# Optimization experiments

Hardware: AMD Instinct MI355X
Metric: run time of the kernel (lower is better)

The kernel has to match this reference:

```python
import jax, jax.numpy as jnp
import numpy as np

LEVELS = 2048
TIMESTAMPS = 64
D = 32768
SIG_LO, SIG_HI = -5.0, 5.0
FEAT_IDX = jnp.array([557, 581, 553, 551, 92, 554, 579, 570, 573, 577, 565, 286, 555, 549, 13, 550, 63, 580, 556, 564, 0, 576, 567, 552, 578, 588, 597, 566, 571, 44, 572, 574, 14, 582, 381, 594, 4, 593, 218, 25, 84, 592, 3, 591, 547, 561, 562, 548, 319, 596, 558, 563, 87, 65, 599, 17, 88, 2, 49, 309, 6, 81, 15, 590, 589, 43, 273, 420, 546, 568, 400, 277, 202, 287, 434, 435, 423, 431, 301, 417, 412, 205, 179, 327, 176, 442, 172, 450, 391, 163, 154, 480, 485, 490, 491, 498, 503, 507, 509, 452, 239, 388, 219, 303, 292, 310, 316, 320, 322, 324, 326, 330, 336, 263, 262, 339, 340, 256, 345, 347], dtype=jnp.int32)


def _bipolar(k, shape):
    # torchhd MAP hypervectors are random +/-1
    return jnp.where(jax.random.bernoulli(k, 0.5, shape), 1.0, -1.0).astype(jnp.float32)


def _level_idx(x, low, high, n):
    # torchhd value_to_index: linear map of [low, high] onto {0, ..., n-1}
    return jnp.clip(jnp.round((x - low) / (high - low) * (n - 1)), 0, n - 1).astype(jnp.int32)


def setup_inputs() -> dict:
    key = jax.random.key(0)
    ks = jax.random.split(key, 7)
    inp = jax.random.normal(ks[0], (TIMESTAMPS, 4), dtype=jnp.float32) * 2.0
    feat = jax.random.normal(ks[1], (600,), dtype=jnp.float32)
    Wx = _bipolar(ks[2], (LEVELS, D))
    Wy = _bipolar(ks[3], (LEVELS, D))
    Wz = _bipolar(ks[4], (LEVELS, D))
    Wt = _bipolar(ks[5], (TIMESTAMPS, D))
    keys = _bipolar(ks[6], (120, D))
    return {"input": inp, "feat": feat, "Wx": Wx, "Wy": Wy, "Wz": Wz, "Wt": Wt, "keys": keys}


def reference(input, feat, Wx, Wy, Wz, Wt, keys):
    # Level-embedding lookups for the clamped x/y/z accelerometer signals
    xl = Wx[_level_idx(jnp.clip(input[:, 1], SIG_LO, SIG_HI), SIG_LO, SIG_HI, LEVELS)]  # [W, D]
    yl = Wy[_level_idx(jnp.clip(input[:, 2], SIG_LO, SIG_HI), SIG_LO, SIG_HI, LEVELS)]
    zl = Wz[_level_idx(jnp.clip(input[:, 3], SIG_LO, SIG_HI), SIG_LO, SIG_HI, LEVELS)]
    window = input.shape[0]
    t = jnp.arange(window, dtype=jnp.float32)
    tl = Wt[_level_idx(t, 0.0, float(TIMESTAMPS), TIMESTAMPS)]  # [W, D]
    sample_hvs = (xl + yl + zl) * tl                            # [W, D]
    sample_hv = jnp.prod(sample_hvs, axis=0)                    # multibind -> [D]
    # DensityFlocet: key-value binding of 120 gathered features with thermometer (flocet) value codes
    fv = jnp.clip(feat[FEAT_IDX], -1.0, 1.0)                    # [120]
    fidx = jnp.round((fv + 1.0) * 0.5 * D).astype(jnp.int32)    # threshold per feature
    therm = jnp.where(jnp.arange(D)[None, :] < fidx[:, None], 1.0, -1.0)  # [120, D]
    feat_hv = jnp.sum(keys * therm, axis=0)                     # multiset(bind) -> [D]
    combined = sample_hv + feat_hv + sample_hv * feat_hv
    return jnp.where(combined > 0, 1.0, -1.0).reshape(-1)       # hard_quantize + flatten
```

## Files before the change

kernel.cpp:

```cpp
#include <hip/hip_runtime.h>

#define D_DIM 32768
#define NT 64
#define NKEYS 120
#define TPB 1024
#define DB 128
#define NW 16

__constant__ int c_feat_idx[NKEYS] = {
    557, 581, 553, 551, 92, 554, 579, 570, 573, 577,
    565, 286, 555, 549, 13, 550, 63, 580, 556, 564,
    0, 576, 567, 552, 578, 588, 597, 566, 571, 44,
    572, 574, 14, 582, 381, 594, 4, 593, 218, 25,
    84, 592, 3, 591, 547, 561, 562, 548, 319, 596,
    558, 563, 87, 65, 599, 17, 88, 2, 49, 309,
    6, 81, 15, 590, 589, 43, 273, 420, 546, 568,
    400, 277, 202, 287, 434, 435, 423, 431, 301, 417,
    412, 205, 179, 327, 176, 442, 172, 450, 391, 163,
    154, 480, 485, 490, 491, 498, 503, 507, 509, 452,
    239, 388, 219, 303, 292, 310, 316, 320, 322, 324,
    326, 330, 336, 263, 262, 339, 340, 256, 345, 347};

__device__ __forceinline__ int level_idx(float x) {
    x = fminf(fmaxf(x, -5.0f), 5.0f);
    float v = (x + 5.0f) / 10.0f * 2047.0f;
    int i = (int)rintf(v);
    return min(max(i, 0), 2047);
}

__global__ __launch_bounds__(TPB) void hdc_encode_kernel(
    const float* __restrict__ input,
    const float* __restrict__ feat,
    const float* __restrict__ Wx,
    const float* __restrict__ Wy,
    const float* __restrict__ Wz,
    const float* __restrict__ Wt,
    const float* __restrict__ keys,
    float* __restrict__ out)
{
    __shared__ int   s_idx[4][NT];
    __shared__ int   s_fidx[NKEYS];
    __shared__ int   s_meta[NW][DB];
    __shared__ float s_f[NW][DB];

    const int tid = threadIdx.x;

    if (tid < NT) {
        float x = input[tid * 4 + 1];
        float y = input[tid * 4 + 2];
        float z = input[tid * 4 + 3];
        s_idx[0][tid] = level_idx(x);
        s_idx[1][tid] = level_idx(y);
        s_idx[2][tid] = level_idx(z);
        float tv = (float)tid;
        int it = (int)rintf(tv / 64.0f * 63.0f);
        s_idx[3][tid] = min(max(it, 0), NT - 1);
    } else if (tid < NT + NKEYS) {
        int j = tid - NT;
        float fv = feat[c_feat_idx[j]];
        fv = fminf(fmaxf(fv, -1.0f), 1.0f);
        s_fidx[j] = (int)rintf((fv + 1.0f) * 0.5f * 32768.0f);
    }
    __syncthreads();

    const int wave = __builtin_amdgcn_readfirstlane(tid >> 6);
    const int lane = tid & 63;
    const int d0 = blockIdx.x * DB + lane * 2;

    unsigned sg0 = 0u, sg1 = 0u;
    int a30 = 0, a31 = 0;
    const int t0 = wave * 4;
#pragma unroll
    for (int k = 0; k < 4; ++k) {
        int t = t0 + k;
        int ix = __builtin_amdgcn_readfirstlane(s_idx[0][t]);
        int iy = __builtin_amdgcn_readfirstlane(s_idx[1][t]);
        int iz = __builtin_amdgcn_readfirstlane(s_idx[2][t]);
        int it = __builtin_amdgcn_readfirstlane(s_idx[3][t]);
        float2 x = *(const float2*)(Wx + ((size_t)ix << 15) + d0);
        float2 y = *(const float2*)(Wy + ((size_t)iy << 15) + d0);
        float2 z = *(const float2*)(Wz + ((size_t)iz << 15) + d0);
        float2 w = *(const float2*)(Wt + ((size_t)it << 15) + d0);
        float sA = x.x + y.x + z.x;
        float sB = x.y + y.y + z.y;
        sg0 ^= __float_as_uint(sA * w.x);
        sg1 ^= __float_as_uint(sB * w.y);
        a30 |= (fabsf(sA) > 2.0f) ? 1 : 0;
        a31 |= (fabsf(sB) > 2.0f) ? 1 : 0;
    }

    float f0 = 0.0f, f1 = 0.0f;
    if (wave < 8) {
        const int j0 = wave * 8;
#pragma unroll
        for (int k = 0; k < 8; ++k) {
            int j = j0 + k;
            int fx = __builtin_amdgcn_readfirstlane(s_fidx[j]);
            float2 kv = *(const float2*)(keys + ((size_t)j << 15) + d0);
            f0 += (d0 < fx) ? kv.x : -kv.x;
            f1 += (d0 + 1 < fx) ? kv.y : -kv.y;
        }
    } else {
        const int j0 = 64 + (wave - 8) * 7;
#pragma unroll
        for (int k = 0; k < 7; ++k) {
            int j = j0 + k;
            int fx = __builtin_amdgcn_readfirstlane(s_fidx[j]);
            float2 kv = *(const float2*)(keys + ((size_t)j << 15) + d0);
            f0 += (d0 < fx) ? kv.x : -kv.x;
            f1 += (d0 + 1 < fx) ? kv.y : -kv.y;
        }
    }

    const int col = lane * 2;
    s_meta[wave][col]     = (int)(sg0 >> 31) | (a30 << 8);
    s_meta[wave][col + 1] = (int)(sg1 >> 31) | (a31 << 8);
    s_f[wave][col]     = f0;
    s_f[wave][col + 1] = f1;
    __syncthreads();

    if (tid < DB) {
        int msum = 0;
        float f = 0.0f;
#pragma unroll
        for (int w2 = 0; w2 < NW; ++w2) {
            msum += s_meta[w2][tid];
            f    += s_f[w2][tid];
        }
        bool neg  = (msum & 1) != 0;
        bool any3 = (msum & 0xFF00) != 0;
        float o;
        if (f >= 0.0f) o = neg ? -1.0f : 1.0f;
        else           o = (neg && any3) ? 1.0f : -1.0f;
        out[blockIdx.x * DB + tid] = o;
    }
}

extern "C" void kernel_launch(void* const* d_in, const int* in_sizes, int n_in,
                              void* d_out, int out_size, void* d_ws, size_t ws_size,
                              hipStream_t stream) {
    const float* input = (const float*)d_in[0];
    const float* feat  = (const float*)d_in[1];
    const float* Wx    = (const float*)d_in[2];
    const float* Wy    = (const float*)d_in[3];
    const float* Wz    = (const float*)d_in[4];
    const float* Wt    = (const float*)d_in[5];
    const float* keys  = (const float*)d_in[6];
    float* out = (float*)d_out;

    dim3 grid(D_DIM / DB);
    dim3 block(TPB);
    hipLaunchKernelGGL(hdc_encode_kernel, grid, block, 0, stream,
                       input, feat, Wx, Wy, Wz, Wt, keys, out);
}
```

Before: 13.79 us.

## Compute indices per wave in registers and batch all gathers before arithmetic

Removes the shared-memory index precompute stage and its barrier: each wave now computes its own level and threshold indices directly from global input. All row loads for the embedding and key tables are issued up front into register arrays before any accumulation, so more memory requests are in flight at once. In exchange, index arithmetic and the small input and feature reads are repeated by every wave of every block, and register pressure rises.

New measurement: 14.84 us. 1.08x slower.

```diff
diff --git a/kernel.cpp b/kernel.cpp
--- a/kernel.cpp
+++ b/kernel.cpp
@@ -38,77 +38,77 @@
     const float* __restrict__ keys,
     float* __restrict__ out)
 {
-    __shared__ int   s_idx[4][NT];
-    __shared__ int   s_fidx[NKEYS];
     __shared__ int   s_meta[NW][DB];
     __shared__ float s_f[NW][DB];
 
-    const int tid = threadIdx.x;
-
-    if (tid < NT) {
-        float x = input[tid * 4 + 1];
-        float y = input[tid * 4 + 2];
-        float z = input[tid * 4 + 3];
-        s_idx[0][tid] = level_idx(x);
-        s_idx[1][tid] = level_idx(y);
-        s_idx[2][tid] = level_idx(z);
-        float tv = (float)tid;
-        int it = (int)rintf(tv / 64.0f * 63.0f);
-        s_idx[3][tid] = min(max(it, 0), NT - 1);
-    } else if (tid < NT + NKEYS) {
-        int j = tid - NT;
-        float fv = feat[c_feat_idx[j]];
-        fv = fminf(fmaxf(fv, -1.0f), 1.0f);
-        s_fidx[j] = (int)rintf((fv + 1.0f) * 0.5f * 32768.0f);
-    }
-    __syncthreads();
-
+    const int tid  = threadIdx.x;
     const int wave = __builtin_amdgcn_readfirstlane(tid >> 6);
     const int lane = tid & 63;
     const int d0 = blockIdx.x * DB + lane * 2;
 
+    int rowx[4], rowy[4], rowz[4], rowt[4];
+#pragma unroll
+    for (int k = 0; k < 4; ++k) {
+        int t = wave * 4 + k;
+        float x = input[t * 4 + 1];
+        float y = input[t * 4 + 2];
+        float z = input[t * 4 + 3];
+        rowx[k] = __builtin_amdgcn_readfirstlane(level_idx(x));
+        rowy[k] = __builtin_amdgcn_readfirstlane(level_idx(y));
+        rowz[k] = __builtin_amdgcn_readfirstlane(level_idx(z));
+        float tv = (float)t;
+        int it = (int)rintf(tv / 64.0f * 63.0f);
+        rowt[k] = __builtin_amdgcn_readfirstlane(min(max(it, 0), NT - 1));
+    }
+
+    const int nk = (wave < 8) ? 8 : 7;
+    const int j0 = (wave < 8) ? wave * 8 : 64 + (wave - 8) * 7;
+    int fxv[8];
+#pragma unroll
+    for (int k = 0; k < 8; ++k) {
+        if (k < nk) {
+            float fv = feat[c_feat_idx[j0 + k]];
+            fv = fminf(fmaxf(fv, -1.0f), 1.0f);
+            fxv[k] = __builtin_amdgcn_readfirstlane((int)rintf((fv + 1.0f) * 0.5f * 32768.0f));
+        } else {
+            fxv[k] = 0;
+        }
+    }
+
+    float2 sx[4], sy[4], sz[4], st[4];
+#pragma unroll
+    for (int k = 0; k < 4; ++k) {
+        sx[k] = *(const float2*)(Wx + ((size_t)rowx[k] << 15) + d0);
+        sy[k] = *(const float2*)(Wy + ((size_t)rowy[k] << 15) + d0);
+        sz[k] = *(const float2*)(Wz + ((size_t)rowz[k] << 15) + d0);
+        st[k] = *(const float2*)(Wt + ((size_t)rowt[k] << 15) + d0);
+    }
+    float2 kv[8];
+#pragma unroll
+    for (int k = 0; k < 8; ++k) {
+        if (k < nk)
+            kv[k] = *(const float2*)(keys + ((size_t)(j0 + k) << 15) + d0);
+    }
+
     unsigned sg0 = 0u, sg1 = 0u;
     int a30 = 0, a31 = 0;
-    const int t0 = wave * 4;
 #pragma unroll
     for (int k = 0; k < 4; ++k) {
-        int t = t0 + k;
-        int ix = __builtin_amdgcn_readfirstlane(s_idx[0][t]);
-        int iy = __builtin_amdgcn_readfirstlane(s_idx[1][t]);
-        int iz = __builtin_amdgcn_readfirstlane(s_idx[2][t]);
-        int it = __builtin_amdgcn_readfirstlane(s_idx[3][t]);
-        float2 x = *(const float2*)(Wx + ((size_t)ix << 15) + d0);
-        float2 y = *(const float2*)(Wy + ((size_t)iy << 15) + d0);
-        float2 z = *(const float2*)(Wz + ((size_t)iz << 15) + d0);
-        float2 w = *(const float2*)(Wt + ((size_t)it << 15) + d0);
-        float sA = x.x + y.x + z.x;
-        float sB = x.y + y.y + z.y;
-        sg0 ^= __float_as_uint(sA * w.x);
-        sg1 ^= __float_as_uint(sB * w.y);
+        float sA = sx[k].x + sy[k].x + sz[k].x;
+        float sB = sx[k].y + sy[k].y + sz[k].y;
+        sg0 ^= __float_as_uint(sA * st[k].x);
+        sg1 ^= __float_as_uint(sB * st[k].y);
         a30 |= (fabsf(sA) > 2.0f) ? 1 : 0;
         a31 |= (fabsf(sB) > 2.0f) ? 1 : 0;
     }
 
     float f0 = 0.0f, f1 = 0.0f;
-    if (wave < 8) {
-        const int j0 = wave * 8;
 #pragma unroll
-        for (int k = 0; k < 8; ++k) {
-            int j = j0 + k;
-            int fx = __builtin_amdgcn_readfirstlane(s_fidx[j]);
-            float2 kv = *(const float2*)(keys + ((size_t)j << 15) + d0);
-            f0 += (d0 < fx) ? kv.x : -kv.x;
-            f1 += (d0 + 1 < fx) ? kv.y : -kv.y;
-        }
-    } else {
-        const int j0 = 64 + (wave - 8) * 7;
-#pragma unroll
-        for (int k = 0; k < 7; ++k) {
-            int j = j0 + k;
-            int fx = __builtin_amdgcn_readfirstlane(s_fidx[j]);
-            float2 kv = *(const float2*)(keys + ((size_t)j << 15) + d0);
-            f0 += (d0 < fx) ? kv.x : -kv.x;
-            f1 += (d0 + 1 < fx) ? kv.y : -kv.y;
+    for (int k = 0; k < 8; ++k) {
+        if (k < nk) {
+            int fx = fxv[k];
+            f0 += (d0 < fx)     ? kv[k].x : -kv[k].x;
+            f1 += (d0 + 1 < fx) ? kv[k].y : -kv[k].y;
         }
     }
 
```

## Split reduction across four blocks per chunk with a separate combine kernel

Applied to the files above, without the earlier changes.

Each 128-column chunk is now processed by four 512-thread blocks, each covering 16 timestamps and 30 keys. Their partial sign/count and feature sums go to workspace, and a second kernel combines them and quantizes. Each wave computes its level indices directly instead of through a shared-memory prologue and barrier, which removes one sync. This raises block count and occupancy, at the cost of an extra kernel launch and a workspace write/read round trip. The any3 flag becomes a count so partial results can be added together.

Result: slower. 15.88 us (+15.2%).

```diff
diff --git a/kernel.cpp b/kernel.cpp
--- a/kernel.cpp
+++ b/kernel.cpp
@@ -3,9 +3,10 @@
 #define D_DIM 32768
 #define NT 64
 #define NKEYS 120
-#define TPB 1024
-#define DB 128
-#define NW 16
+#define RS 4
+#define CHUNK 128
+#define K1_TPB 512
+#define K1_WAVES 8
 
 __constant__ int c_feat_idx[NKEYS] = {
     557, 581, 553, 551, 92, 554, 579, 570, 573, 577,
@@ -28,7 +29,7 @@
     return min(max(i, 0), 2047);
 }
 
-__global__ __launch_bounds__(TPB) void hdc_encode_kernel(
+__global__ __launch_bounds__(K1_TPB, 8) void hdc_partial_kernel(
     const float* __restrict__ input,
     const float* __restrict__ feat,
     const float* __restrict__ Wx,
@@ -36,78 +37,59 @@
     const float* __restrict__ Wz,
     const float* __restrict__ Wt,
     const float* __restrict__ keys,
-    float* __restrict__ out)
+    int*   __restrict__ ws_m,
+    float* __restrict__ ws_f)
 {
-    __shared__ int   s_idx[4][NT];
-    __shared__ int   s_fidx[NKEYS];
-    __shared__ int   s_meta[NW][DB];
-    __shared__ float s_f[NW][DB];
+    __shared__ int   s_meta[K1_WAVES][CHUNK];
+    __shared__ float s_f[K1_WAVES][CHUNK];
 
-    const int tid = threadIdx.x;
+    const int tid   = threadIdx.x;
+    const int wave  = __builtin_amdgcn_readfirstlane(tid >> 6);
+    const int lane  = tid & 63;
+    const int chunk = blockIdx.x >> 2;
+    const int rg    = blockIdx.x & 3;
+    const int d0    = chunk * CHUNK + lane * 2;
 
-    if (tid < NT) {
-        float x = input[tid * 4 + 1];
-        float y = input[tid * 4 + 2];
-        float z = input[tid * 4 + 3];
-        s_idx[0][tid] = level_idx(x);
-        s_idx[1][tid] = level_idx(y);
-        s_idx[2][tid] = level_idx(z);
-        float tv = (float)tid;
-        int it = (int)rintf(tv / 64.0f * 63.0f);
-        s_idx[3][tid] = min(max(it, 0), NT - 1);
-    } else if (tid < NT + NKEYS) {
-        int j = tid - NT;
-        float fv = feat[c_feat_idx[j]];
-        fv = fminf(fmaxf(fv, -1.0f), 1.0f);
-        s_fidx[j] = (int)rintf((fv + 1.0f) * 0.5f * 32768.0f);
+    const int t0 = rg * 16 + wave * 2;
+    int rx[2], ry[2], rz[2], rt[2];
+#pragma unroll
+    for (int k = 0; k < 2; ++k) {
+        int t = t0 + k;
+        rx[k] = __builtin_amdgcn_readfirstlane(level_idx(input[t * 4 + 1]));
+        ry[k] = __builtin_amdgcn_readfirstlane(level_idx(input[t * 4 + 2]));
+        rz[k] = __builtin_amdgcn_readfirstlane(level_idx(input[t * 4 + 3]));
+        int it = (int)rintf((float)t / 64.0f * 63.0f);
+        rt[k] = __builtin_amdgcn_readfirstlane(min(max(it, 0), NT - 1));
     }
-    __syncthreads();
-
-    const int wave = __builtin_amdgcn_readfirstlane(tid >> 6);
-    const int lane = tid & 63;
-    const int d0 = blockIdx.x * DB + lane * 2;
+    const int nk = (wave < 6) ? 4 : 3;
+    const int j0 = rg * 30 + ((wave < 6) ? wave * 4 : 24 + (wave - 6) * 3);
 
     unsigned sg0 = 0u, sg1 = 0u;
     int a30 = 0, a31 = 0;
-    const int t0 = wave * 4;
 #pragma unroll
-    for (int k = 0; k < 4; ++k) {
-        int t = t0 + k;
-        int ix = __builtin_amdgcn_readfirstlane(s_idx[0][t]);
-        int iy = __builtin_amdgcn_readfirstlane(s_idx[1][t]);
-        int iz = __builtin_amdgcn_readfirstlane(s_idx[2][t]);
-        int it = __builtin_amdgcn_readfirstlane(s_idx[3][t]);
-        float2 x = *(const float2*)(Wx + ((size_t)ix << 15) + d0);
-        float2 y = *(const float2*)(Wy + ((size_t)iy << 15) + d0);
-        float2 z = *(const float2*)(Wz + ((size_t)iz << 15) + d0);
-        float2 w = *(const float2*)(Wt + ((size_t)it << 15) + d0);
+    for (int k = 0; k < 2; ++k) {
+        float2 x = *(const float2*)(Wx + ((size_t)rx[k] << 15) + d0);
+        float2 y = *(const float2*)(Wy + ((size_t)ry[k] << 15) + d0);
+        float2 z = *(const float2*)(Wz + ((size_t)rz[k] << 15) + d0);
+        float2 w = *(const float2*)(Wt + ((size_t)rt[k] << 15) + d0);
         float sA = x.x + y.x + z.x;
         float sB = x.y + y.y + z.y;
         sg0 ^= __float_as_uint(sA * w.x);
         sg1 ^= __float_as_uint(sB * w.y);
-        a30 |= (fabsf(sA) > 2.0f) ? 1 : 0;
-        a31 |= (fabsf(sB) > 2.0f) ? 1 : 0;
+        a30 += (fabsf(sA) > 2.0f) ? 1 : 0;
+        a31 += (fabsf(sB) > 2.0f) ? 1 : 0;
     }
 
     float f0 = 0.0f, f1 = 0.0f;
-    if (wave < 8) {
-        const int j0 = wave * 8;
 #pragma unroll
-        for (int k = 0; k < 8; ++k) {
+    for (int k = 0; k < 4; ++k) {
+        if (k < nk) {
             int j = j0 + k;
-            int fx = __builtin_amdgcn_readfirstlane(s_fidx[j]);
+            float fv = feat[c_feat_idx[j]];
+            fv = fminf(fmaxf(fv, -1.0f), 1.0f);
+            int fx = __builtin_amdgcn_readfirstlane((int)rintf((fv + 1.0f) * 0.5f * 32768.0f));
             float2 kv = *(const float2*)(keys + ((size_t)j << 15) + d0);
-            f0 += (d0 < fx) ? kv.x : -kv.x;
-            f1 += (d0 + 1 < fx) ? kv.y : -kv.y;
-        }
-    } else {
-        const int j0 = 64 + (wave - 8) * 7;
-#pragma unroll
-        for (int k = 0; k < 7; ++k) {
-            int j = j0 + k;
-            int fx = __builtin_amdgcn_readfirstlane(s_fidx[j]);
-            float2 kv = *(const float2*)(keys + ((size_t)j << 15) + d0);
-            f0 += (d0 < fx) ? kv.x : -kv.x;
+            f0 += (d0 < fx)     ? kv.x : -kv.x;
             f1 += (d0 + 1 < fx) ? kv.y : -kv.y;
         }
     }
@@ -119,21 +101,34 @@
     s_f[wave][col + 1] = f1;
     __syncthreads();
 
-    if (tid < DB) {
+    if (tid < CHUNK) {
         int msum = 0;
         float f = 0.0f;
 #pragma unroll
-        for (int w2 = 0; w2 < NW; ++w2) {
+        for (int w2 = 0; w2 < K1_WAVES; ++w2) {
             msum += s_meta[w2][tid];
             f    += s_f[w2][tid];
         }
-        bool neg  = (msum & 1) != 0;
-        bool any3 = (msum & 0xFF00) != 0;
-        float o;
-        if (f >= 0.0f) o = neg ? -1.0f : 1.0f;
-        else           o = (neg && any3) ? 1.0f : -1.0f;
-        out[blockIdx.x * DB + tid] = o;
+        int d = chunk * CHUNK + tid;
+        ws_m[rg * D_DIM + d] = msum;
+        ws_f[rg * D_DIM + d] = f;
     }
+}
+
+__global__ __launch_bounds__(256) void hdc_combine_kernel(
+    const int*   __restrict__ ws_m,
+    const float* __restrict__ ws_f,
+    float* __restrict__ out)
+{
+    int d = blockIdx.x * 256 + threadIdx.x;
+    int m = ws_m[d] + ws_m[D_DIM + d] + ws_m[2 * D_DIM + d] + ws_m[3 * D_DIM + d];
+    float f = ws_f[d] + ws_f[D_DIM + d] + ws_f[2 * D_DIM + d] + ws_f[3 * D_DIM + d];
+    bool neg  = (m & 1) != 0;
+    bool any3 = (m >> 8) != 0;
+    float o;
+    if (f >= 0.0f) o = neg ? -1.0f : 1.0f;
+    else           o = (neg && any3) ? 1.0f : -1.0f;
+    out[d] = o;
 }
 
 extern "C" void kernel_launch(void* const* d_in, const int* in_sizes, int n_in,
@@ -148,8 +143,16 @@
     const float* keys  = (const float*)d_in[6];
     float* out = (float*)d_out;
 
-    dim3 grid(D_DIM / DB);
-    dim3 block(TPB);
-    hipLaunchKernelGGL(hdc_encode_kernel, grid, block, 0, stream,
-                       input, feat, Wx, Wy, Wz, Wt, keys, out);
+    int*   ws_m = (int*)d_ws;
+    float* ws_f = (float*)((char*)d_ws + (size_t)RS * D_DIM * 4);
+
+    dim3 grid1(D_DIM / CHUNK * RS);
+    dim3 block1(K1_TPB);
+    hipLaunchKernelGGL(hdc_partial_kernel, grid1, block1, 0, stream,
+                       input, feat, Wx, Wy, Wz, Wt, keys, ws_m, ws_f);
+
+    dim3 grid2(D_DIM / 256);
+    dim3 block2(256);
+    hipLaunchKernelGGL(hdc_combine_kernel, grid2, block2, 0, stream,
+                       ws_m, ws_f, out);
 }
```
